# Optimization experiments

Hardware: AMD Instinct MI355X
Metric: run time of the kernel (lower is better)

The kernel has to match this reference:

```python
import jax, jax.numpy as jnp
import numpy as np

N = 100000   # nodes
E = 1600000  # directed edges
D_IN, D_HID, D_OUT, N_CLS = 128, 256, 128, 10
EPS = 1e-5


def gcn_conv(x, W, b, src, dst, n):
    # PyG GCNConv: h = XW, add self loops, sym-normalize, scatter-add to dst, + bias
    h = x @ W
    loop = jnp.arange(n)
    src_f = jnp.concatenate([src, loop])
    dst_f = jnp.concatenate([dst, loop])
    deg = jax.ops.segment_sum(jnp.ones(src_f.shape[0], h.dtype), dst_f, num_segments=n)
    dinv = jnp.where(deg > 0, jax.lax.rsqrt(deg), jnp.zeros_like(deg))
    norm = dinv[src_f] * dinv[dst_f]                    # [E+N]
    out = jax.ops.segment_sum(h[src_f] * norm[:, None], dst_f, num_segments=n)
    return out + b


def batchnorm(x, gamma, beta):
    # training-mode BatchNorm1d (batch statistics, biased variance)
    mu = x.mean(0)
    var = x.var(0)
    return gamma * (x - mu) * jax.lax.rsqrt(var + EPS) + beta


def setup_inputs() -> dict:
    key = jax.random.key(0)
    ks = jax.random.split(key, 12)
    x = jax.random.normal(ks[0], (N, D_IN), jnp.float32)
    edge_index = jax.random.randint(ks[1], (2, E), 0, N, dtype=jnp.int64)
    def lin(k, fi, fo):
        s = 1.0 / np.sqrt(fi)
        return jax.random.uniform(k, (fi, fo), jnp.float32, -s, s)
    return {
        "x": x, "edge_index": edge_index,
        "W1": lin(ks[2], D_IN, D_HID), "b1": jnp.zeros(D_HID, jnp.float32),
        "g1": jnp.ones(D_HID, jnp.float32), "beta1": jnp.zeros(D_HID, jnp.float32),
        "W2": lin(ks[3], D_HID, D_HID), "b2": jnp.zeros(D_HID, jnp.float32),
        "g2": jnp.ones(D_HID, jnp.float32), "beta2": jnp.zeros(D_HID, jnp.float32),
        "W3": lin(ks[4], D_HID, D_OUT), "b3": jnp.zeros(D_OUT, jnp.float32),
        "g3": jnp.ones(D_OUT, jnp.float32), "beta3": jnp.zeros(D_OUT, jnp.float32),
        "Wout": lin(ks[5], D_OUT, N_CLS), "bout": jnp.zeros(N_CLS, jnp.float32),
    }


def reference(x, edge_index, W1, b1, g1, beta1, W2, b2, g2, beta2,
              W3, b3, g3, beta3, Wout, bout):
    src, dst = edge_index[0], edge_index[1]
    h = jax.nn.relu(batchnorm(gcn_conv(x, W1, b1, src, dst, N), g1, beta1))
    h = jax.nn.relu(batchnorm(gcn_conv(h, W2, b2, src, dst, N), g2, beta2))
    h = jax.nn.relu(batchnorm(gcn_conv(h, W3, b3, src, dst, N), g3, beta3))
    return h @ Wout + bout
```

## Files before the change

kernel.cpp:

```cpp
#include <hip/hip_runtime.h>
#include <hip/hip_fp16.h>
#include <cstdint>
#include <cstddef>

#define EPS_BN 1e-5f
#define NSLICE 16
#define NCHUNK 16

static inline int cdiv(int a, int b) { return (a + b - 1) / b; }

using half8   = __attribute__((ext_vector_type(8))) _Float16;
using floatx4 = __attribute__((ext_vector_type(4))) float;

__device__ __forceinline__ float atomAddF(float* p, float v) {
    return unsafeAtomicAdd(p, v);
}


__global__ __launch_bounds__(256) void k_hist(const int* __restrict__ dst, int E, int EL,
                                              int NBLK, int NBUCK, int* __restrict__ H) {
    __shared__ int h[256];
    int t = threadIdx.x;
    h[t] = 0;
    __syncthreads();
    int base = blockIdx.x * 4096;
#pragma unroll
    for (int j = 0; j < 16; ++j) {
        int e = base + j * 256 + t;
        if (e < EL) {
            int d = (e < E) ? dst[e] : (e - E);
            atomicAdd(&h[d >> 9], 1);
        }
    }
    __syncthreads();
    if (t < NBUCK) H[t * NBLK + blockIdx.x] = h[t];
}

__global__ __launch_bounds__(256) void k_scan_reduce(const int* __restrict__ in, int m,
                                                     int* __restrict__ bsum) {
    int base = blockIdx.x * 1024;
    int t = threadIdx.x;
    int s = 0;
#pragma unroll
    for (int i = 0; i < 4; ++i) {
        int idx = base + t * 4 + i;
        if (idx < m) s += in[idx];
    }
    __shared__ int sm[256];
    sm[t] = s;
    __syncthreads();
    for (int off = 128; off > 0; off >>= 1) {
        if (t < off) sm[t] += sm[t + off];
        __syncthreads();
    }
    if (t == 0) bsum[blockIdx.x] = sm[0];
}

__global__ void k_scan_bsum(int* __restrict__ bsum, int nb) {
    if (threadIdx.x == 0 && blockIdx.x == 0) {
        int acc = 0;
        for (int i = 0; i < nb; ++i) { int v = bsum[i]; bsum[i] = acc; acc += v; }
    }
}

__global__ __launch_bounds__(256) void k_scan_final(const int* __restrict__ in, int m,
                                                    const int* __restrict__ bsum,
                                                    int* __restrict__ outS) {
    int base = blockIdx.x * 1024;
    int t = threadIdx.x;
    int v[4];
    int s = 0;
#pragma unroll
    for (int i = 0; i < 4; ++i) {
        int idx = base + t * 4 + i;
        v[i] = (idx < m) ? in[idx] : 0;
        s += v[i];
    }
    __shared__ int sm[256];
    sm[t] = s;
    __syncthreads();
    for (int off = 1; off < 256; off <<= 1) {
        int x = (t >= off) ? sm[t - off] : 0;
        __syncthreads();
        sm[t] += x;
        __syncthreads();
    }
    int excl = sm[t] - s + bsum[blockIdx.x];
#pragma unroll
    for (int i = 0; i < 4; ++i) {
        int idx = base + t * 4 + i;
        if (idx < m) { outS[idx] = excl; excl += v[i]; }
    }
}

__global__ __launch_bounds__(256) void k_bucket(const int* __restrict__ src,
                                                const int* __restrict__ dst, int E, int EL,
                                                int NBLK, int NBUCK,
                                                const int* __restrict__ S,
                                                unsigned* __restrict__ pairs) {
    __shared__ int cur[256];
    int t = threadIdx.x;
    if (t < NBUCK) cur[t] = S[t * NBLK + blockIdx.x];
    __syncthreads();
    int base = blockIdx.x * 4096;
#pragma unroll
    for (int j = 0; j < 16; ++j) {
        int e = base + j * 256 + t;
        if (e < EL) {
            unsigned s, d;
            if (e < E) { s = (unsigned)src[e]; d = (unsigned)dst[e]; }
            else       { s = d = (unsigned)(e - E); }
            int p = atomicAdd(&cur[d >> 9], 1);
            pairs[p] = ((d & 511u) << 17) | s;
        }
    }
}

__global__ __launch_bounds__(256) void k_build(const unsigned* __restrict__ pairs,
                                               const int* __restrict__ S,
                                               int NBLK, int NBUCK, int n, int EL, int sh,
                                               int* __restrict__ endoff,
                                               float* __restrict__ dinv,
                                               int* __restrict__ csr) {
    int b = blockIdx.x;
    int nbase = b << 9;
    int bstart = S[b * NBLK];
    int bend = (b == NBUCK - 1) ? EL : S[(b + 1) * NBLK];
    int t = threadIdx.x;
    __shared__ int sdeg[8192];
    __shared__ int scur[8192];
    __shared__ int stmp[256];
#pragma unroll
    for (int i = 0; i < 32; ++i) sdeg[t + i * 256] = 0;
    __syncthreads();
    for (int e = bstart + t; e < bend; e += 256) {
        unsigned p = pairs[e];
        int key = (int)((p >> 17) << 4) | (int)((p & 0x1FFFFu) >> sh);
        atomicAdd(&sdeg[key], 1);
    }
    __syncthreads();
    int loc[32];
    int ls = 0;
#pragma unroll
    for (int i = 0; i < 32; ++i) { loc[i] = sdeg[t * 32 + i]; ls += loc[i]; }
    stmp[t] = ls;
    __syncthreads();
    for (int off = 1; off < 256; off <<= 1) {
        int x = (t >= off) ? stmp[t - off] : 0;
        __syncthreads();
        stmp[t] += x;
        __syncthreads();
    }
    int run = bstart + stmp[t] - ls;
    int d0 = 0, d1 = 0;
    int v0 = nbase + 2 * t, v1 = v0 + 1;
#pragma unroll
    for (int i = 0; i < 32; ++i) {
        scur[t * 32 + i] = run;
        int e_ = run + loc[i];
        int v = (i < 16) ? v0 : v1;
        if (v < n) endoff[(size_t)v * NCHUNK + (i & 15)] = e_;
        run = e_;
        if (i < 16) d0 += loc[i]; else d1 += loc[i];
    }
    if (v0 < n) dinv[v0] = rsqrtf((float)d0);
    if (v1 < n) dinv[v1] = rsqrtf((float)d1);
    __syncthreads();
    for (int e = bstart + t; e < bend; e += 256) {
        unsigned p = pairs[e];
        int key = (int)((p >> 17) << 4) | (int)((p & 0x1FFFFu) >> sh);
        int pos = atomicAdd(&scur[key], 1);
        csr[pos] = (int)(p & 0x1FFFFu);
    }
}

__global__ __launch_bounds__(256) void k_prep(const float* __restrict__ x,
                                              const float* __restrict__ dinv,
                                              const float* __restrict__ W1,
                                              const float* __restrict__ W2,
                                              const float* __restrict__ W3,
                                              __half* __restrict__ xh,
                                              __half* __restrict__ Wt1,
                                              __half* __restrict__ Wt2,
                                              __half* __restrict__ Wt3,
                                              float* __restrict__ stats, int n) {
    int idx = blockIdx.x * 256 + threadIdx.x;
    int nx = n * 16;
    if (idx < nx) {
        int row = idx >> 4;
        float dv = dinv[row];
        const float4* p = (const float4*)x + (size_t)idx * 2;
        float4 a = p[0], b = p[1];
        uint4 o; __half2* oh = (__half2*)&o;
        oh[0] = __floats2half2_rn(a.x * dv, a.y * dv);
        oh[1] = __floats2half2_rn(a.z * dv, a.w * dv);
        oh[2] = __floats2half2_rn(b.x * dv, b.y * dv);
        oh[3] = __floats2half2_rn(b.z * dv, b.w * dv);
        ((uint4*)xh)[idx] = o;
        return;
    }
    int r = idx - nx;
    if (r < 32768) {
        int k = r >> 8, c = r & 255;
        Wt1[c * 128 + k] = __float2half(W1[r]);
    } else if (r < 98304) {
        int r2 = r - 32768;
        int k = r2 >> 8, c = r2 & 255;
        Wt2[c * 256 + k] = __float2half(W2[r2]);
    } else if (r < 131072) {
        int r2 = r - 98304;
        int k = r2 >> 7, c = r2 & 127;
        Wt3[c * 256 + k] = __float2half(W3[r2]);
    } else if (r < 131072 + NSLICE * 256 * 6) {
        stats[r - 131072] = 0.f;
    }
}

__device__ __forceinline__ void acc8(float* acc, uint4 d) {
    const __half2* h = (const __half2*)&d;
#pragma unroll
    for (int j = 0; j < 4; ++j) {
        float2 f = __half22float2(h[j]);
        acc[2 * j] += f.x; acc[2 * j + 1] += f.y;
    }
}

template<int D>
__device__ __forceinline__ void gseg(const __half* __restrict__ Pb,
                                     const int* __restrict__ csr,
                                     int i, int end, float* acc) {
    int rem = (end - i) & 3;
    if (rem & 2) {
        uint4 d0 = *(const uint4*)(Pb + (size_t)csr[i] * D);
        uint4 d1 = *(const uint4*)(Pb + (size_t)csr[i + 1] * D);
        acc8(acc, d0); acc8(acc, d1);
        i += 2;
    }
    if (rem & 1) {
        uint4 d0 = *(const uint4*)(Pb + (size_t)csr[i] * D);
        acc8(acc, d0);
        ++i;
    }
    if (i < end) {
        uint4 a[4];
#pragma unroll
        for (int u = 0; u < 4; ++u)
            a[u] = *(const uint4*)(Pb + (size_t)csr[i + u] * D);
        for (i += 4; i < end; i += 4) {
            uint4 b[4];
#pragma unroll
            for (int u = 0; u < 4; ++u)
                b[u] = *(const uint4*)(Pb + (size_t)csr[i + u] * D);
#pragma unroll
            for (int u = 0; u < 4; ++u) acc8(acc, a[u]);
#pragma unroll
            for (int u = 0; u < 4; ++u) a[u] = b[u];
        }
#pragma unroll
        for (int u = 0; u < 4; ++u) acc8(acc, a[u]);
    }
}

template<int D, bool STATS>
__global__ __launch_bounds__(256, 8) void k_gather6(const int* __restrict__ csr,
                                                    const int* __restrict__ endoff,
                                                    const __half* __restrict__ P,
                                                    const float* __restrict__ dinv,
                                                    __half* __restrict__ S, int n,
                                                    float* __restrict__ sums,
                                                    float* __restrict__ sqs) {
    constexpr int NSL = D / 64;
    __shared__ float red[STATS ? 2048 : 1];
    int bid = blockIdx.x;
    int x8 = bid & 7;
    int slice, gidx;
    if (NSL == 4) { slice = x8 >> 1; gidx = (bid >> 3) * 2 + (x8 & 1); }
    else          { slice = x8 >> 2; gidx = (bid >> 3) * 4 + (x8 & 3); }
    int Gn = (n + 31) >> 5;
    if (gidx >= Gn) return;
    int t = threadIdx.x;
    int lane = t & 7;
    int sub = t >> 3;
    int v = gidx * 32 + sub;
    int c0 = (int)((wall_clock64() / 100ull) & (unsigned long long)(NCHUNK - 1));
    const __half* Pb = P + (size_t)slice * 64 + lane * 8;
    float ov[8];
#pragma unroll
    for (int j = 0; j < 8; ++j) ov[j] = 0.f;
    if (v < n) {
        float acc[8] = {};
        size_t i0 = (size_t)v * NCHUNK;
        int beg = (i0 == 0) ? 0 : endoff[i0 - 1];
        int end = endoff[i0 + NCHUNK - 1];
        int mid = (c0 == 0) ? beg : endoff[i0 + c0 - 1];
        gseg<D>(Pb, csr, mid, end, acc);
        gseg<D>(Pb, csr, beg, mid, acc);
        float dv = dinv[v];
        uint4 o; __half2* oh = (__half2*)&o;
#pragma unroll
        for (int j = 0; j < 4; ++j) {
            float a0 = acc[2 * j] * dv, a1 = acc[2 * j + 1] * dv;
            oh[j] = __floats2half2_rn(a0, a1);
            ov[2 * j] = a0; ov[2 * j + 1] = a1;
        }
        *(uint4*)(S + (size_t)v * D + slice * 64 + lane * 8) = o;
    }
    if (STATS) {
        int shard = bid & (NSLICE - 1);
#pragma unroll
        for (int j = 0; j < 8; ++j) red[t * 8 + j] = ov[j];
        __syncthreads();
        if (t < 64) {
            int ln = t >> 3, j = t & 7;
            float ts = 0.f;
#pragma unroll
            for (int s = 0; s < 32; ++s) ts += red[(s * 8 + ln) * 8 + j];
            atomAddF(&sums[shard * 256 + slice * 64 + t], ts);
        }
        __syncthreads();
#pragma unroll
        for (int j = 0; j < 8; ++j) red[t * 8 + j] = ov[j] * ov[j];
        __syncthreads();
        if (t < 64) {
            int ln = t >> 3, j = t & 7;
            float tq = 0.f;
#pragma unroll
            for (int s = 0; s < 32; ++s) tq += red[(s * 8 + ln) * 8 + j];
            atomAddF(&sqs[shard * 256 + slice * 64 + t], tq);
        }
    }
}

template<int K, int NC, bool SCALE, bool BNIN, bool STATS>
__global__ __launch_bounds__(2 * NC) void k_gemm_mfma(const __half* __restrict__ A,
                                                   const __half* __restrict__ Wt,
                                                   const float* __restrict__ dinv,
                                                   const float* __restrict__ isum,
                                                   const float* __restrict__ isq,
                                                   const float* __restrict__ g,
                                                   const float* __restrict__ beta,
                                                   float* __restrict__ osum,
                                                   float* __restrict__ osq,
                                                   __half* __restrict__ C, int n) {
    constexpr int THREADS = 2 * NC;
    constexpr int CW = NC / 64;
    constexpr int LDA = 40;
    __shared__ _Float16 As[128 * LDA];
    __shared__ _Float16 Bs[NC * LDA];
    __shared__ float ssc[BNIN ? K : 1];
    __shared__ float ssh[BNIN ? K : 1];
    __shared__ float scs[STATS ? NC : 1];
    __shared__ float scq[STATS ? NC : 1];
    int tid = threadIdx.x;
    if (BNIN) {
        float nf = (float)n;
        for (int i = tid; i < K; i += THREADS) {
            float su = 0.f, sq = 0.f;
#pragma unroll
            for (int s = 0; s < NSLICE; ++s) {
                su += isum[s * 256 + i];
                sq += isq[s * 256 + i];
            }
            float mu = su / nf;
            float var = sq / nf - mu * mu;
            float sc = g[i] * rsqrtf(var + EPS_BN);
            ssc[i] = sc; ssh[i] = beta[i] - mu * sc;
        }
        __syncthreads();
    }
    int wave = tid >> 6, lane = tid & 63;
    int wr = wave / CW, wc = wave % CW;
    int q = lane >> 4, l16 = lane & 15;
    int row0 = blockIdx.x * 128;
    floatx4 acc[4][4];
#pragma unroll
    for (int r = 0; r < 4; ++r)
#pragma unroll
        for (int c = 0; c < 4; ++c) acc[r][c] = (floatx4)0.0f;

    for (int k0 = 0; k0 < K; k0 += 32) {
        constexpr int AIT = 512 / THREADS;
#pragma unroll
        for (int i = 0; i < AIT; ++i) {
            int s = tid + i * THREADS;
            int r = s >> 2, ks = s & 3;
            uint4 d = *(const uint4*)(A + (size_t)(row0 + r) * K + k0 + ks * 8);
            if (BNIN) {
                const __half2* h = (const __half2*)&d;
                uint4 o; __half2* oh = (__half2*)&o;
                int kb = k0 + ks * 8;
#pragma unroll
                for (int j = 0; j < 4; ++j) {
                    float2 f = __half22float2(h[j]);
                    float y0 = fmaxf(0.f, f.x * ssc[kb + 2 * j]     + ssh[kb + 2 * j]);
                    float y1 = fmaxf(0.f, f.y * ssc[kb + 2 * j + 1] + ssh[kb + 2 * j + 1]);
                    oh[j] = __floats2half2_rn(y0, y1);
                }
                d = o;
            }
            *(uint4*)&As[r * LDA + ks * 8] = d;
        }
        constexpr int BIT = NC * 4 / THREADS;
#pragma unroll
        for (int i = 0; i < BIT; ++i) {
            int s = tid + i * THREADS;
            int r = s >> 2, ks = s & 3;
            uint4 d = *(const uint4*)(Wt + (size_t)r * K + k0 + ks * 8);
            *(uint4*)&Bs[r * LDA + ks * 8] = d;
        }
        __syncthreads();
        half8 af[4], bf[4];
#pragma unroll
        for (int r = 0; r < 4; ++r)
            af[r] = *(const half8*)&As[(wr * 64 + r * 16 + l16) * LDA + q * 8];
#pragma unroll
        for (int c = 0; c < 4; ++c)
            bf[c] = *(const half8*)&Bs[(wc * 64 + c * 16 + l16) * LDA + q * 8];
#pragma unroll
        for (int r = 0; r < 4; ++r)
#pragma unroll
            for (int c = 0; c < 4; ++c)
                acc[r][c] = __builtin_amdgcn_mfma_f32_16x16x32_f16(af[r], bf[c], acc[r][c], 0, 0, 0);
        __syncthreads();
    }
    float colsum[4] = {};
    float colsq[4]  = {};
#pragma unroll
    for (int r = 0; r < 4; ++r) {
#pragma unroll
        for (int reg = 0; reg < 4; ++reg) {
            int grow = row0 + wr * 64 + r * 16 + q * 4 + reg;
            float sc = 1.f;
            if (SCALE) sc = (grow < n) ? dinv[grow] : 0.f;
            __half* cp = C + (size_t)grow * NC + wc * 64 + l16;
#pragma unroll
            for (int c = 0; c < 4; ++c) {
                float v = acc[r][c][reg] * sc;
                cp[c * 16] = __float2half(v);
                if (STATS && grow < n) { colsum[c] += v; colsq[c] += v * v; }
            }
        }
    }
    if (STATS) {
        if (tid < NC) { scs[tid] = 0.f; scq[tid] = 0.f; }
        __syncthreads();
#pragma unroll
        for (int c = 0; c < 4; ++c) {
            atomicAdd(&scs[wc * 64 + c * 16 + l16], colsum[c]);
            atomicAdd(&scq[wc * 64 + c * 16 + l16], colsq[c]);
        }
        __syncthreads();
        if (tid < NC) {
            int slice = blockIdx.x & (NSLICE - 1);
            atomAddF(&osum[slice * 256 + tid], scs[tid]);
            atomAddF(&osq[slice * 256 + tid], scq[tid]);
        }
    }
}

__global__ __launch_bounds__(256) void k_out(const __half* __restrict__ H,
                                             const float* __restrict__ sums,
                                             const float* __restrict__ sqs,
                                             const float* __restrict__ g,
                                             const float* __restrict__ beta,
                                             const float* __restrict__ Wout,
                                             const float* __restrict__ bout,
                                             float* __restrict__ out, int n) {
    __shared__ float Wl[128 * 10];
    __shared__ float bl[10];
    __shared__ float osc[128];
    __shared__ float osh[128];
    __shared__ float red[256 * 10];
    int tid = threadIdx.x;
    for (int i = tid; i < 1280; i += 256) Wl[i] = Wout[i];
    if (tid < 10) bl[tid] = bout[tid];
    if (tid < 128) {
        float nf = (float)n;
        float su = 0.f, sq = 0.f;
#pragma unroll
        for (int s = 0; s < NSLICE; ++s) {
            su += sums[s * 256 + tid];
            sq += sqs[s * 256 + tid];
        }
        float mu = su / nf;
        float var = sq / nf - mu * mu;
        float sc = g[tid] * rsqrtf(var + EPS_BN);
        osc[tid] = sc; osh[tid] = beta[tid] - mu * sc;
    }
    __syncthreads();
    int rl = tid >> 1;
    int h2 = tid & 1;
    int r = blockIdx.x * 128 + rl;
    float p[10] = {};
    if (r < n) {
        const __half* a = H + (size_t)r * 128 + h2 * 64;
#pragma unroll 8
        for (int k = 0; k < 64; ++k) {
            int col = h2 * 64 + k;
            float av = fmaxf(0.f, __half2float(a[k]) * osc[col] + osh[col]);
            const float* wr = Wl + col * 10;
#pragma unroll
            for (int c = 0; c < 10; ++c) p[c] += av * wr[c];
        }
    }
    float* rr = red + (size_t)tid * 10;
#pragma unroll
    for (int c = 0; c < 10; ++c) rr[c] = p[c];
    __syncthreads();
    if (h2 == 0 && r < n) {
        const float* rb = red + (size_t)tid * 10;
#pragma unroll
        for (int c = 0; c < 10; ++c) {
            out[(size_t)r * 10 + c] = rb[c] + rb[10 + c] + bl[c];
        }
    }
}

extern "C" void kernel_launch(void* const* d_in, const int* in_sizes, int n_in,
                              void* d_out, int out_size, void* d_ws, size_t ws_size,
                              hipStream_t stream) {
    const float* x    = (const float*)d_in[0];
    const int*   ei   = (const int*)d_in[1];
    const float* W1   = (const float*)d_in[2];
    const float* g1   = (const float*)d_in[4];
    const float* be1  = (const float*)d_in[5];
    const float* W2   = (const float*)d_in[6];
    const float* g2   = (const float*)d_in[8];
    const float* be2  = (const float*)d_in[9];
    const float* W3   = (const float*)d_in[10];
    const float* g3   = (const float*)d_in[12];
    const float* be3  = (const float*)d_in[13];
    const float* Wout = (const float*)d_in[14];
    const float* bout = (const float*)d_in[15];
    float* out = (float*)d_out;

    int n = in_sizes[0] / 128;
    int E = in_sizes[1] / 2;
    const int* esrc = ei;
    const int* edst = ei + E;
    int EL = E + n;
    int npad = cdiv(n, 128) * 128;
    int NBLK = cdiv(EL, 4096);
    int NBUCK = (n + 511) >> 9;
    if (NBUCK > 256) return;
    int m = NBUCK * NBLK;
    int nb2 = cdiv(m, 1024);
    int sh = 0;
    while ((NCHUNK << sh) < n) ++sh;

    const size_t align = 256;
    auto al = [&](size_t s) { return (s + align - 1) & ~(align - 1); };
    size_t n4  = al((size_t)n * 4 + 512);
    size_t nE8 = al((size_t)n * NCHUNK * 4 + 512);

    const size_t statsLayer = (size_t)NSLICE * 256 * 2 * 4;
    const size_t statsTotal = statsLayer * 3;

    char* ws = (char*)d_ws;
    size_t o_end   = 0;
    size_t o_dinv  = o_end + nE8;
    size_t o_stats = o_dinv + n4;
    size_t o_bsum  = o_stats + statsTotal;
    size_t o_H     = o_bsum + 1024;
    size_t o_Hs    = o_H + al((size_t)m * 4);
    size_t o_csr   = o_Hs + al((size_t)m * 4);
    size_t o_pairs = o_csr + al((size_t)EL * 4);
    size_t o_w1    = o_pairs + al((size_t)EL * 4);
    size_t o_w2    = o_w1 + al(256 * 128 * 2);
    size_t o_w3    = o_w2 + al(256 * 256 * 2);
    size_t o_A128a = o_w3 + al(128 * 256 * 2);
    size_t o_A128b = o_A128a + al((size_t)npad * 128 * 2);
    size_t o_A256a = o_A128b + al((size_t)npad * 128 * 2);
    size_t o_A256b = o_A256a + al((size_t)npad * 256 * 2);
    size_t need    = o_A256b + (size_t)npad * 256 * 2;
    if (ws_size < need) return;

    int*      endoff = (int*)(ws + o_end);
    float*    dinv   = (float*)(ws + o_dinv);
    float*    stats  = (float*)(ws + o_stats);
    float*    sums1  = stats;
    float*    sqs1   = sums1 + NSLICE * 256;
    float*    sums2  = (float*)(ws + o_stats + statsLayer);
    float*    sqs2   = sums2 + NSLICE * 256;
    float*    sums3  = (float*)(ws + o_stats + 2 * statsLayer);
    float*    sqs3   = sums3 + NSLICE * 256;
    int*      bsum   = (int*)(ws + o_bsum);
    int*      H      = (int*)(ws + o_H);
    int*      Hs     = (int*)(ws + o_Hs);
    int*      csr    = (int*)(ws + o_csr);
    unsigned* pairs  = (unsigned*)(ws + o_pairs);
    __half*   Wt1    = (__half*)(ws + o_w1);
    __half*   Wt2    = (__half*)(ws + o_w2);
    __half*   Wt3    = (__half*)(ws + o_w3);
    __half*   xh     = (__half*)(ws + o_A128a);
    __half*   S3     = (__half*)(ws + o_A128a);
    __half*   G1     = (__half*)(ws + o_A128b);
    __half*   P3     = (__half*)(ws + o_A128b);
    __half*   P1     = (__half*)(ws + o_A256a);
    __half*   S2     = (__half*)(ws + o_A256a);
    __half*   P2     = (__half*)(ws + o_A256b);

    k_hist<<<NBLK, 256, 0, stream>>>(edst, E, EL, NBLK, NBUCK, H);
    k_scan_reduce<<<nb2, 256, 0, stream>>>(H, m, bsum);
    k_scan_bsum<<<1, 64, 0, stream>>>(bsum, nb2);
    k_scan_final<<<nb2, 256, 0, stream>>>(H, m, bsum, Hs);
    k_bucket<<<NBLK, 256, 0, stream>>>(esrc, edst, E, EL, NBLK, NBUCK, Hs, pairs);
    k_build<<<NBUCK, 256, 0, stream>>>(pairs, Hs, NBLK, NBUCK, n, EL, sh, endoff, dinv, csr);

    int prepTotal = n * 16 + 131072 + NSLICE * 256 * 6;
    k_prep<<<cdiv(prepTotal, 256), 256, 0, stream>>>(
        x, dinv, W1, W2, W3, xh, Wt1, Wt2, Wt3, stats, n);

    int Gn = (n + 31) >> 5;
    int grid128 = 8 * cdiv(Gn, 4);
    int grid256 = 8 * cdiv(Gn, 2);

    k_gather6<128, false><<<grid128, 256, 0, stream>>>(
        csr, endoff, xh, dinv, G1, n, nullptr, nullptr);
    k_gemm_mfma<128, 256, false, false, true><<<dim3(npad / 128), 512, 0, stream>>>(
        G1, Wt1, dinv, nullptr, nullptr, nullptr, nullptr, sums1, sqs1, P1, n);

    k_gemm_mfma<256, 256, true, true, false><<<dim3(npad / 128), 512, 0, stream>>>(
        P1, Wt2, dinv, sums1, sqs1, g1, be1, nullptr, nullptr, P2, n);
    k_gather6<256, true><<<grid256, 256, 0, stream>>>(
        csr, endoff, P2, dinv, S2, n, sums2, sqs2);

    k_gemm_mfma<256, 128, true, true, false><<<dim3(npad / 128), 256, 0, stream>>>(
        S2, Wt3, dinv, sums2, sqs2, g2, be2, nullptr, nullptr, P3, n);
    k_gather6<128, true><<<grid128, 256, 0, stream>>>(
        csr, endoff, P3, dinv, S3, n, sums3, sqs3);

    k_out<<<cdiv(n, 128), 256, 0, stream>>>(S3, sums3, sqs3, g3, be3, Wout, bout, out, n);
}
```

Before: 540.0 us.

## Pad CSR rows to multiples of eight with a zero dummy node

Each node's neighbor list in the CSR is padded to a multiple of eight using index n, which points to an explicitly zeroed row in every feature buffer. The per-node 16-chunk end-offset table becomes a compact begin/end pair. The gather kernel drops its remainder handling and the clock-based rotated start, and runs a fixed 8-wide software-pipelined load loop. This removes branchy tail code and keeps more loads in flight. The cost is up to seven wasted loads per node, plus extra CSR workspace and zeroed pad rows.

```diff
diff --git a/kernel.cpp b/kernel.cpp
--- a/kernel.cpp
+++ b/kernel.cpp
@@ -6,6 +6,7 @@
 #define EPS_BN 1e-5f
 #define NSLICE 16
 #define NCHUNK 16
+#define BPAD 3584
 
 static inline int cdiv(int a, int b) { return (a + b - 1) / b; }
 
@@ -119,13 +120,14 @@
 __global__ __launch_bounds__(256) void k_build(const unsigned* __restrict__ pairs,
                                                const int* __restrict__ S,
                                                int NBLK, int NBUCK, int n, int EL, int sh,
-                                               int* __restrict__ endoff,
+                                               int* __restrict__ boff,
                                                float* __restrict__ dinv,
                                                int* __restrict__ csr) {
     int b = blockIdx.x;
     int nbase = b << 9;
     int bstart = S[b * NBLK];
     int bend = (b == NBUCK - 1) ? EL : S[(b + 1) * NBLK];
+    int cbase = bstart + b * BPAD;
     int t = threadIdx.x;
     __shared__ int sdeg[8192];
     __shared__ int scur[8192];
@@ -140,9 +142,14 @@
     }
     __syncthreads();
     int loc[32];
-    int ls = 0;
-#pragma unroll
-    for (int i = 0; i < 32; ++i) { loc[i] = sdeg[t * 32 + i]; ls += loc[i]; }
+    int d0 = 0, d1 = 0;
+#pragma unroll
+    for (int i = 0; i < 32; ++i) {
+        loc[i] = sdeg[t * 32 + i];
+        if (i < 16) d0 += loc[i]; else d1 += loc[i];
+    }
+    int p0 = (-d0) & 7, p1 = (-d1) & 7;
+    int ls = d0 + p0 + d1 + p1;
     stmp[t] = ls;
     __syncthreads();
     for (int off = 1; off < 256; off <<= 1) {
@@ -151,20 +158,28 @@
         stmp[t] += x;
         __syncthreads();
     }
-    int run = bstart + stmp[t] - ls;
-    int d0 = 0, d1 = 0;
+    int run = cbase + stmp[t] - ls;
     int v0 = nbase + 2 * t, v1 = v0 + 1;
-#pragma unroll
-    for (int i = 0; i < 32; ++i) {
-        scur[t * 32 + i] = run;
-        int e_ = run + loc[i];
-        int v = (i < 16) ? v0 : v1;
-        if (v < n) endoff[(size_t)v * NCHUNK + (i & 15)] = e_;
-        run = e_;
-        if (i < 16) d0 += loc[i]; else d1 += loc[i];
-    }
-    if (v0 < n) dinv[v0] = rsqrtf((float)d0);
-    if (v1 < n) dinv[v1] = rsqrtf((float)d1);
+    int beg0 = run;
+#pragma unroll
+    for (int i = 0; i < 16; ++i) { scur[t * 32 + i] = run; run += loc[i]; }
+    int re0 = run;
+    run += p0;
+    int beg1 = run;
+#pragma unroll
+    for (int i = 16; i < 32; ++i) { scur[t * 32 + i] = run; run += loc[i]; }
+    int re1 = run;
+    run += p1;
+    if (v0 < n) {
+        boff[2 * v0] = beg0; boff[2 * v0 + 1] = beg1;
+        dinv[v0] = rsqrtf((float)d0);
+        for (int j = 0; j < p0; ++j) csr[re0 + j] = n;
+    }
+    if (v1 < n) {
+        boff[2 * v1] = beg1; boff[2 * v1 + 1] = re1 + p1;
+        dinv[v1] = rsqrtf((float)d1);
+        for (int j = 0; j < p1; ++j) csr[re1 + j] = n;
+    }
     __syncthreads();
     for (int e = bstart + t; e < bend; e += 256) {
         unsigned p = pairs[e];
@@ -199,7 +214,12 @@
         ((uint4*)xh)[idx] = o;
         return;
     }
-    int r = idx - nx;
+    if (idx < nx + 16) {
+        uint4 z = {0u, 0u, 0u, 0u};
+        ((uint4*)xh)[idx] = z;
+        return;
+    }
+    int r = idx - nx - 16;
     if (r < 32768) {
         int k = r >> 8, c = r & 255;
         Wt1[c * 128 + k] = __float2half(W1[r]);
@@ -225,45 +245,9 @@
     }
 }
 
-template<int D>
-__device__ __forceinline__ void gseg(const __half* __restrict__ Pb,
-                                     const int* __restrict__ csr,
-                                     int i, int end, float* acc) {
-    int rem = (end - i) & 3;
-    if (rem & 2) {
-        uint4 d0 = *(const uint4*)(Pb + (size_t)csr[i] * D);
-        uint4 d1 = *(const uint4*)(Pb + (size_t)csr[i + 1] * D);
-        acc8(acc, d0); acc8(acc, d1);
-        i += 2;
-    }
-    if (rem & 1) {
-        uint4 d0 = *(const uint4*)(Pb + (size_t)csr[i] * D);
-        acc8(acc, d0);
-        ++i;
-    }
-    if (i < end) {
-        uint4 a[4];
-#pragma unroll
-        for (int u = 0; u < 4; ++u)
-            a[u] = *(const uint4*)(Pb + (size_t)csr[i + u] * D);
-        for (i += 4; i < end; i += 4) {
-            uint4 b[4];
-#pragma unroll
-            for (int u = 0; u < 4; ++u)
-                b[u] = *(const uint4*)(Pb + (size_t)csr[i + u] * D);
-#pragma unroll
-            for (int u = 0; u < 4; ++u) acc8(acc, a[u]);
-#pragma unroll
-            for (int u = 0; u < 4; ++u) a[u] = b[u];
-        }
-#pragma unroll
-        for (int u = 0; u < 4; ++u) acc8(acc, a[u]);
-    }
-}
-
 template<int D, bool STATS>
-__global__ __launch_bounds__(256, 8) void k_gather6(const int* __restrict__ csr,
-                                                    const int* __restrict__ endoff,
+__global__ __launch_bounds__(256, 8) void k_gather7(const int* __restrict__ csr,
+                                                    const int* __restrict__ boff,
                                                     const __half* __restrict__ P,
                                                     const float* __restrict__ dinv,
                                                     __half* __restrict__ S, int n,
@@ -276,25 +260,33 @@
     int slice, gidx;
     if (NSL == 4) { slice = x8 >> 1; gidx = (bid >> 3) * 2 + (x8 & 1); }
     else          { slice = x8 >> 2; gidx = (bid >> 3) * 4 + (x8 & 3); }
-    int Gn = (n + 31) >> 5;
+    int Gn = (n + 32) >> 5;
     if (gidx >= Gn) return;
     int t = threadIdx.x;
     int lane = t & 7;
     int sub = t >> 3;
     int v = gidx * 32 + sub;
-    int c0 = (int)((wall_clock64() / 100ull) & (unsigned long long)(NCHUNK - 1));
     const __half* Pb = P + (size_t)slice * 64 + lane * 8;
     float ov[8];
 #pragma unroll
     for (int j = 0; j < 8; ++j) ov[j] = 0.f;
     if (v < n) {
         float acc[8] = {};
-        size_t i0 = (size_t)v * NCHUNK;
-        int beg = (i0 == 0) ? 0 : endoff[i0 - 1];
-        int end = endoff[i0 + NCHUNK - 1];
-        int mid = (c0 == 0) ? beg : endoff[i0 + c0 - 1];
-        gseg<D>(Pb, csr, mid, end, acc);
-        gseg<D>(Pb, csr, beg, mid, acc);
+        int2 be = *(const int2*)(boff + 2 * v);
+        int i = be.x, end = be.y;
+        uint4 a[8];
+#pragma unroll
+        for (int u = 0; u < 8; ++u)
+            a[u] = *(const uint4*)(Pb + (size_t)csr[i + u] * D);
+        for (i += 8; i < end; i += 8) {
+#pragma unroll
+            for (int u = 0; u < 8; ++u) {
+                acc8(acc, a[u]);
+                a[u] = *(const uint4*)(Pb + (size_t)csr[i + u] * D);
+            }
+        }
+#pragma unroll
+        for (int u = 0; u < 8; ++u) acc8(acc, a[u]);
         float dv = dinv[v];
         uint4 o; __half2* oh = (__half2*)&o;
 #pragma unroll
@@ -304,6 +296,9 @@
             ov[2 * j] = a0; ov[2 * j + 1] = a1;
         }
         *(uint4*)(S + (size_t)v * D + slice * 64 + lane * 8) = o;
+    } else if (v == n) {
+        uint4 z = {0u, 0u, 0u, 0u};
+        *(uint4*)(S + (size_t)v * D + slice * 64 + lane * 8) = z;
     }
     if (STATS) {
         int shard = bid & (NSLICE - 1);
@@ -539,7 +534,7 @@
     const int* esrc = ei;
     const int* edst = ei + E;
     int EL = E + n;
-    int npad = cdiv(n, 128) * 128;
+    int npad = cdiv(n + 1, 128) * 128;
     int NBLK = cdiv(EL, 4096);
     int NBUCK = (n + 511) >> 9;
     if (NBUCK > 256) return;
@@ -551,20 +546,22 @@
     const size_t align = 256;
     auto al = [&](size_t s) { return (s + align - 1) & ~(align - 1); };
     size_t n4  = al((size_t)n * 4 + 512);
-    size_t nE8 = al((size_t)n * NCHUNK * 4 + 512);
+    size_t nB  = al((size_t)n * 8 + 512);
 
     const size_t statsLayer = (size_t)NSLICE * 256 * 2 * 4;
     const size_t statsTotal = statsLayer * 3;
 
+    size_t csrN = (size_t)EL + (size_t)NBUCK * BPAD;
+
     char* ws = (char*)d_ws;
-    size_t o_end   = 0;
-    size_t o_dinv  = o_end + nE8;
+    size_t o_boff  = 0;
+    size_t o_dinv  = o_boff + nB;
     size_t o_stats = o_dinv + n4;
     size_t o_bsum  = o_stats + statsTotal;
     size_t o_H     = o_bsum + 1024;
     size_t o_Hs    = o_H + al((size_t)m * 4);
     size_t o_csr   = o_Hs + al((size_t)m * 4);
-    size_t o_pairs = o_csr + al((size_t)EL * 4);
+    size_t o_pairs = o_csr + al(csrN * 4);
     size_t o_w1    = o_pairs + al((size_t)EL * 4);
     size_t o_w2    = o_w1 + al(256 * 128 * 2);
     size_t o_w3    = o_w2 + al(256 * 256 * 2);
@@ -575,7 +572,7 @@
     size_t need    = o_A256b + (size_t)npad * 256 * 2;
     if (ws_size < need) return;
 
-    int*      endoff = (int*)(ws + o_end);
+    int*      boff   = (int*)(ws + o_boff);
     float*    dinv   = (float*)(ws + o_dinv);
     float*    stats  = (float*)(ws + o_stats);
     float*    sums1  = stats;
@@ -605,30 +602,30 @@
     k_scan_bsum<<<1, 64, 0, stream>>>(bsum, nb2);
     k_scan_final<<<nb2, 256, 0, stream>>>(H, m, bsum, Hs);
     k_bucket<<<NBLK, 256, 0, stream>>>(esrc, edst, E, EL, NBLK, NBUCK, Hs, pairs);
-    k_build<<<NBUCK, 256, 0, stream>>>(pairs, Hs, NBLK, NBUCK, n, EL, sh, endoff, dinv, csr);
-
-    int prepTotal = n * 16 + 131072 + NSLICE * 256 * 6;
+    k_build<<<NBUCK, 256, 0, stream>>>(pairs, Hs, NBLK, NBUCK, n, EL, sh, boff, dinv, csr);
+
+    int prepTotal = n * 16 + 16 + 131072 + NSLICE * 256 * 6;
     k_prep<<<cdiv(prepTotal, 256), 256, 0, stream>>>(
         x, dinv, W1, W2, W3, xh, Wt1, Wt2, Wt3, stats, n);
 
-    int Gn = (n + 31) >> 5;
+    int Gn = (n + 32) >> 5;
     int grid128 = 8 * cdiv(Gn, 4);
     int grid256 = 8 * cdiv(Gn, 2);
 
-    k_gather6<128, false><<<grid128, 256, 0, stream>>>(
-        csr, endoff, xh, dinv, G1, n, nullptr, nullptr);
+    k_gather7<128, false><<<grid128, 256, 0, stream>>>(
+        csr, boff, xh, dinv, G1, n, nullptr, nullptr);
     k_gemm_mfma<128, 256, false, false, true><<<dim3(npad / 128), 512, 0, stream>>>(
         G1, Wt1, dinv, nullptr, nullptr, nullptr, nullptr, sums1, sqs1, P1, n);
 
     k_gemm_mfma<256, 256, true, true, false><<<dim3(npad / 128), 512, 0, stream>>>(
         P1, Wt2, dinv, sums1, sqs1, g1, be1, nullptr, nullptr, P2, n);
-    k_gather6<256, true><<<grid256, 256, 0, stream>>>(
-        csr, endoff, P2, dinv, S2, n, sums2, sqs2);
+    k_gather7<256, true><<<grid256, 256, 0, stream>>>(
+        csr, boff, P2, dinv, S2, n, sums2, sqs2);
 
     k_gemm_mfma<256, 128, true, true, false><<<dim3(npad / 128), 256, 0, stream>>>(
         S2, Wt3, dinv, sums2, sqs2, g2, be2, nullptr, nullptr, P3, n);
-    k_gather6<128, true><<<grid128, 256, 0, stream>>>(
-        csr, endoff, P3, dinv, S3, n, sums3, sqs3);
+    k_gather7<128, true><<<grid128, 256, 0, stream>>>(
+        csr, boff, P3, dinv, S3, n, sums3, sqs3);
 
     k_out<<<cdiv(n, 128), 256, 0, stream>>>(S3, sums3, sqs3, g3, be3, Wout, bout, out, n);
 }
```

Result: slower. 638.7 us (+18.3%).
